# Kernel tuning notes

Measured on AMD Instinct MI355X. Metric: run time of the kernel, lower is better.

Reference implementation:

```python
import jax, jax.numpy as jnp
import numpy as np

N = 50000          # num nodes
E = 800000         # num edges (avg degree 16)
R = 8              # num relations
IN = 128
H0 = 256
H1 = 64


def _w(key, shape, fan_in):
    return jax.random.normal(key, shape, dtype=jnp.float32) * (1.0 / np.sqrt(fan_in))


def setup_inputs() -> dict:
    key = jax.random.key(0)
    ks = jax.random.split(key, 16)
    x = jax.random.normal(ks[0], (N, IN), dtype=jnp.float32)
    edge_index = jax.random.randint(ks[1], (2, E), 0, N, dtype=jnp.int64)
    edge_type = jax.random.randint(ks[2], (E,), 0, R, dtype=jnp.int64)
    return {
        "x": x,
        "edge_index": edge_index,
        "edge_type": edge_type,
        # RGCNConv params: per-relation weights [R, in, out], root weight [in, out], bias [out]
        "W1": _w(ks[3], (R, IN, H0), IN), "root1": _w(ks[4], (IN, H0), IN), "b1": jnp.zeros((H0,), jnp.float32),
        "W2": _w(ks[5], (R, H0, H0), H0), "root2": _w(ks[6], (H0, H0), H0), "b2": jnp.zeros((H0,), jnp.float32),
        "W3": _w(ks[7], (R, H0, H0), H0), "root3": _w(ks[8], (H0, H0), H0), "b3": jnp.zeros((H0,), jnp.float32),
        "W4": _w(ks[9], (R, H0, H1), H0), "root4": _w(ks[10], (H0, H1), H0), "b4": jnp.zeros((H1,), jnp.float32),
    }


def rgcn_layer(x, edge_index, edge_type, W, root, bias):
    """PyG RGCNConv: out_i = x_i @ root + sum_r (1/|N_r(i)|) sum_{j in N_r(i)} x_j @ W_r + bias.
    Aggregation is linear, so aggregate source features per (relation, dst) first,
    then apply the R small GEMMs — avoids per-edge [E, out] message materialization."""
    src, dst = edge_index[0], edge_index[1]
    seg = edge_type * N + dst                      # combined (relation, dst) segment id
    nseg = R * N
    agg = jax.ops.segment_sum(x[src], seg, num_segments=nseg)          # [R*N, in]
    cnt = jax.ops.segment_sum(jnp.ones((seg.shape[0],), x.dtype), seg, num_segments=nseg)
    agg = agg / jnp.maximum(cnt, 1.0)[:, None]                          # mean per (r, i)
    agg = agg.reshape(R, N, x.shape[1])                                 # [R, N, in]
    return jnp.einsum('rni,rio->no', agg, W) + x @ root + bias


def reference(x, edge_index, edge_type, W1, root1, b1, W2, root2, b2, W3, root3, b3, W4, root4, b4):
    h = jax.nn.relu(rgcn_layer(x, edge_index, edge_type, W1, root1, b1))
    h = jax.nn.relu(rgcn_layer(h, edge_index, edge_type, W2, root2, b2))
    h = jax.nn.relu(rgcn_layer(h, edge_index, edge_type, W3, root3, b3))
    return rgcn_layer(h, edge_index, edge_type, W4, root4, b4)
```

## Files before the change

kernel.cpp:

```cpp
#include <hip/hip_runtime.h>

#define N_NODES 50000
#define N_PAD   50048
#define N_EDGES 800000
#define N_REL   8
#define NSEG    (N_REL * N_NODES)
#define SCAN_NB 391
#define NSTRIPE 391
#define SPX     49

typedef short bf16x8 __attribute__((ext_vector_type(8)));
typedef float f32x4  __attribute__((ext_vector_type(4)));

__device__ __forceinline__ ushort f2bf(float f) {
    union { float f; unsigned u; } c; c.f = f;
    unsigned u = c.u + 0x7fffu + ((c.u >> 16) & 1u);
    return (ushort)(u >> 16);
}
__device__ __forceinline__ void add8(float* s, uint4 v) {
    unsigned u[4] = {v.x, v.y, v.z, v.w};
    #pragma unroll
    for (int k = 0; k < 4; ++k) {
        s[2 * k]     += __uint_as_float(u[k] << 16);
        s[2 * k + 1] += __uint_as_float(u[k] & 0xffff0000u);
    }
}
__device__ __forceinline__ void fma8(float* s, uint4 v, float w) {
    unsigned u[4] = {v.x, v.y, v.z, v.w};
    #pragma unroll
    for (int k = 0; k < 4; ++k) {
        s[2 * k]     = fmaf(__uint_as_float(u[k] << 16),        w, s[2 * k]);
        s[2 * k + 1] = fmaf(__uint_as_float(u[k] & 0xffff0000u), w, s[2 * k + 1]);
    }
}
__device__ __forceinline__ void async16(const ushort* g, ushort* l) {
    __builtin_amdgcn_global_load_lds((const __attribute__((address_space(1))) void*)g,
                                     (__attribute__((address_space(3))) void*)l, 16, 0, 0);
}


__global__ void count_edges(const int* __restrict__ dst, const int* __restrict__ et,
                            int* __restrict__ cnt) {
    int e = blockIdx.x * 256 + threadIdx.x;
    if (e < N_EDGES) atomicAdd(&cnt[dst[e] * N_REL + et[e]], 1);
}

__global__ __launch_bounds__(256) void scan_pass1(const int* __restrict__ cnt,
                                                  int* __restrict__ sums) {
    __shared__ int sc[256];
    int b = blockIdx.x, t = threadIdx.x;
    int base = b * 1024 + t * 4;
    int v = 0;
    #pragma unroll
    for (int i = 0; i < 4; ++i) { int idx = base + i; if (idx < NSEG) v += cnt[idx]; }
    sc[t] = v; __syncthreads();
    for (int off = 1; off < 256; off <<= 1) {
        int x = (t >= off) ? sc[t - off] : 0;
        __syncthreads(); sc[t] += x; __syncthreads();
    }
    if (t == 255) sums[b] = sc[255];
}

__global__ __launch_bounds__(512) void scan_pass2(int* __restrict__ sums, int nb) {
    __shared__ int sc[512];
    int t = threadIdx.x;
    int v = (t < nb) ? sums[t] : 0;
    sc[t] = v; __syncthreads();
    for (int off = 1; off < 512; off <<= 1) {
        int x = (t >= off) ? sc[t - off] : 0;
        __syncthreads(); sc[t] += x; __syncthreads();
    }
    if (t < nb) sums[t] = sc[t] - v;
}

__global__ __launch_bounds__(256) void scan_pass3(const int* __restrict__ cnt,
                                                  const int* __restrict__ sums,
                                                  int* __restrict__ row_ptr) {
    __shared__ int sc[256];
    int b = blockIdx.x, t = threadIdx.x;
    int base = b * 1024 + t * 4;
    int e[4]; int v = 0;
    #pragma unroll
    for (int i = 0; i < 4; ++i) { int idx = base + i; e[i] = (idx < NSEG) ? cnt[idx] : 0; v += e[i]; }
    sc[t] = v; __syncthreads();
    for (int off = 1; off < 256; off <<= 1) {
        int x = (t >= off) ? sc[t - off] : 0;
        __syncthreads(); sc[t] += x; __syncthreads();
    }
    int run = sums[b] + (sc[t] - v);
    #pragma unroll
    for (int i = 0; i < 4; ++i) {
        int idx = base + i;
        if (idx < NSEG) row_ptr[idx] = run;
        run += e[i];
    }
    if (b == 0 && t == 0) row_ptr[NSEG] = N_EDGES;
}

__global__ void place_edges(const int* __restrict__ src, const int* __restrict__ dst,
                            const int* __restrict__ et, const int* __restrict__ row_ptr,
                            int* __restrict__ cnt, int* __restrict__ sorted) {
    int e = blockIdx.x * 256 + threadIdx.x;
    if (e >= N_EDGES) return;
    int r = et[e];
    int key = dst[e] * N_REL + r;
    int old = atomicSub(&cnt[key], 1);
    int r0 = row_ptr[key];
    int c = row_ptr[key + 1] - r0;
    sorted[r0 + old - 1] = src[e] | (r << 17) | (c << 20);
}


__global__ void convert_weights(const float* __restrict__ W, const float* __restrict__ root,
                                ushort* __restrict__ BT, int K, int O, int NPAD) {
    int idx = blockIdx.x * 256 + threadIdx.x;
    if (idx >= NPAD * K) return;
    int col = idx / K, i = idx % K;
    float v = 0.0f;
    if (col < N_REL * O) {
        int r = col / O, o = col % O;
        v = W[((size_t)r * K + i) * O + o];
    } else if (col < (N_REL + 1) * O) {
        v = root[(size_t)i * O + (col - N_REL * O)];
    }
    BT[idx] = f2bf(v);
}

__global__ void f32_to_bf16(const float* __restrict__ in, ushort* __restrict__ out, int n4) {
    int i = blockIdx.x * 256 + threadIdx.x;
    if (i >= n4) return;
    float4 v = ((const float4*)in)[i];
    ushort4 s; s.x = f2bf(v.x); s.y = f2bf(v.y); s.z = f2bf(v.z); s.w = f2bf(v.w);
    ((ushort4*)out)[i] = s;
}

template<int K, int CTS, int NW>
__global__ __launch_bounds__(256)
void gemm_mfma(const ushort* __restrict__ A, const ushort* __restrict__ BT,
               ushort* __restrict__ Y) {
    const int f = blockIdx.x;
    const int g = f & 7, m = f >> 3;
    const int y = g + 8 * (m / CTS);
    const int ct = m % CTS;
    if (y >= NSTRIPE) return;
    const int row0 = y * 128;
    const int col0 = ct * 128;

    __shared__ ushort SMEM[16384];
    const int t = threadIdx.x;
    const int lane = t & 63;
    const int w = t >> 6;
    const int l16 = lane & 15, q = lane >> 4;
    const int wm = (w & 1) * 64, wn = (w >> 1) * 64;

    const int c0i = w * 64 + lane;
    const int c1i = c0i + 256;
    const int r0i = c0i >> 2, r1i = c1i >> 2;
    const int j0i = (c0i & 3) ^ ((r0i >> 1) & 3);
    const int j1i = (c1i & 3) ^ ((r1i >> 1) & 3);
    const size_t ga0 = (size_t)r0i * K + (size_t)j0i * 8;
    const size_t ga1 = (size_t)r1i * K + (size_t)j1i * 8;
    const ushort* Ab = A + (size_t)row0 * K;
    const ushort* Bb = BT + (size_t)col0 * K;

    const int qx = (q ^ ((l16 >> 1) & 3)) * 8;

    f32x4 acc[4][4] = {};

    auto STAGE = [&](int b, int k0) {
        ushort* As = SMEM + b * 8192;
        ushort* Bs = As + 4096;
        async16(Ab + k0 + ga0, &As[w * 512]);
        async16(Ab + k0 + ga1, &As[(w + 4) * 512]);
        async16(Bb + k0 + ga0, &Bs[w * 512]);
        async16(Bb + k0 + ga1, &Bs[(w + 4) * 512]);
    };
    auto COMPUTE = [&](int b) {
        ushort* As = SMEM + b * 8192;
        ushort* Bs = As + 4096;
        bf16x8 a[4], bb[4];
        #pragma unroll
        for (int i = 0; i < 4; ++i) {
            a[i]  = *(const bf16x8*)&As[(wm + i * 16 + l16) * 32 + qx];
            bb[i] = *(const bf16x8*)&Bs[(wn + i * 16 + l16) * 32 + qx];
        }
        #pragma unroll
        for (int i = 0; i < 4; ++i)
            #pragma unroll
            for (int j = 0; j < 4; ++j)
                acc[i][j] = __builtin_amdgcn_mfma_f32_16x16x32_bf16(a[i], bb[j], acc[i][j], 0, 0, 0);
    };

    constexpr int NSTEP = K / 32;
    STAGE(0, 0);
    __syncthreads();
    #pragma unroll
    for (int s = 0; s < NSTEP; ++s) {
        if (s + 1 < NSTEP) STAGE((s + 1) & 1, 32 * (s + 1));
        COMPUTE(s & 1);
        __syncthreads();
    }

    ushort* Ts = &SMEM[w * 32 * 72];
    const int rr = lane >> 3;
    const int cc = (lane & 7) * 8;
    #pragma unroll
    for (int half = 0; half < 2; ++half) {
        #pragma unroll
        for (int i = 0; i < 2; ++i)
            #pragma unroll
            for (int j = 0; j < 4; ++j)
                #pragma unroll
                for (int r = 0; r < 4; ++r)
                    Ts[(i * 16 + q * 4 + r) * 72 + j * 16 + l16] = f2bf(acc[half * 2 + i][j][r]);
        #pragma unroll
        for (int p = 0; p < 4; ++p) {
            int row = p * 8 + rr;
            uint4 v = *(const uint4*)&Ts[row * 72 + cc];
            *(uint4*)(Y + (size_t)(row0 + wm + half * 32 + row) * NW + col0 + wn + cc) = v;
        }
    }
}

template<int O>
__global__ __launch_bounds__(256)
void gather_kernel(const ushort* __restrict__ Y, int NW,
                   const int* __restrict__ row_ptr, const int* __restrict__ sorted,
                   const float* __restrict__ bias,
                   float* __restrict__ out_f32, ushort* __restrict__ out_bf16, int relu) {
    constexpr int TPN = O / 8;
    int d = blockIdx.x * (256 / TPN) + threadIdx.x / TPN;
    if (d >= N_NODES) return;
    int c0 = (threadIdx.x % TPN) * 8;
    int p0 = row_ptr[d * N_REL];
    int p1 = row_ptr[d * N_REL + N_REL];
    float sum[8] = {};
    add8(sum, *(const uint4*)(Y + (size_t)d * NW + N_REL * O + c0));
    #pragma unroll
    for (int k = 0; k < 8; ++k) sum[k] += bias[c0 + k];
    const ushort* Yc = Y + c0;
    #define EDGE_LD(sx) (*(const uint4*)(Yc + (size_t)((sx) & 0x1FFFF) * NW + ((((sx) >> 17) & 7) * O)))
    #define EDGE_W(sx)  (1.0f / (float)((unsigned)(sx) >> 20))
    int e = p0;
    for (; e + 8 <= p1; e += 8) {
        int s0 = sorted[e],     s1 = sorted[e + 1], s2 = sorted[e + 2], s3 = sorted[e + 3];
        int s4 = sorted[e + 4], s5 = sorted[e + 5], s6 = sorted[e + 6], s7 = sorted[e + 7];
        uint4 v0 = EDGE_LD(s0);
        uint4 v1 = EDGE_LD(s1);
        uint4 v2 = EDGE_LD(s2);
        uint4 v3 = EDGE_LD(s3);
        uint4 v4 = EDGE_LD(s4);
        uint4 v5 = EDGE_LD(s5);
        uint4 v6 = EDGE_LD(s6);
        uint4 v7 = EDGE_LD(s7);
        fma8(sum, v0, EDGE_W(s0));
        fma8(sum, v1, EDGE_W(s1));
        fma8(sum, v2, EDGE_W(s2));
        fma8(sum, v3, EDGE_W(s3));
        fma8(sum, v4, EDGE_W(s4));
        fma8(sum, v5, EDGE_W(s5));
        fma8(sum, v6, EDGE_W(s6));
        fma8(sum, v7, EDGE_W(s7));
    }
    if (e + 4 <= p1) {
        int s0 = sorted[e], s1 = sorted[e + 1], s2 = sorted[e + 2], s3 = sorted[e + 3];
        uint4 v0 = EDGE_LD(s0);
        uint4 v1 = EDGE_LD(s1);
        uint4 v2 = EDGE_LD(s2);
        uint4 v3 = EDGE_LD(s3);
        fma8(sum, v0, EDGE_W(s0));
        fma8(sum, v1, EDGE_W(s1));
        fma8(sum, v2, EDGE_W(s2));
        fma8(sum, v3, EDGE_W(s3));
        e += 4;
    }
    for (; e < p1; ++e) {
        int s = sorted[e];
        uint4 v = EDGE_LD(s);
        fma8(sum, v, EDGE_W(s));
    }
    #undef EDGE_LD
    #undef EDGE_W
    if (relu) {
        #pragma unroll
        for (int k = 0; k < 8; ++k) sum[k] = fmaxf(sum[k], 0.0f);
    }
    if (out_bf16) {
        ushort o[8];
        #pragma unroll
        for (int k = 0; k < 8; ++k) o[k] = f2bf(sum[k]);
        *(uint4*)(out_bf16 + (size_t)d * O + c0) = *(const uint4*)o;
    } else {
        float* p = out_f32 + (size_t)d * O + c0;
        *(float4*)p = make_float4(sum[0], sum[1], sum[2], sum[3]);
        *(float4*)(p + 4) = make_float4(sum[4], sum[5], sum[6], sum[7]);
    }
}


extern "C" void kernel_launch(void* const* d_in, const int* in_sizes, int n_in,
                              void* d_out, int out_size, void* d_ws, size_t ws_size,
                              hipStream_t stream) {
    const float* x  = (const float*)d_in[0];
    const int*   ei = (const int*)d_in[1];
    const int*   et = (const int*)d_in[2];
    const float* W[4]  = {(const float*)d_in[3], (const float*)d_in[6], (const float*)d_in[9],  (const float*)d_in[12]};
    const float* RT[4] = {(const float*)d_in[4], (const float*)d_in[7], (const float*)d_in[10], (const float*)d_in[13]};
    const float* BI[4] = {(const float*)d_in[5], (const float*)d_in[8], (const float*)d_in[11], (const float*)d_in[14]};
    const int KS[4] = {128, 256, 256, 256};
    const int NP[4] = {2304, 2304, 2304, 640};
    const int* src = ei;
    const int* dst = ei + N_EDGES;

    char* ws = (char*)d_ws;
    size_t off = 0;
    auto take = [&](size_t bytes) -> char* {
        char* p = ws + off;
        off = (off + bytes + 255) & ~(size_t)255;
        return p;
    };
    int* row_ptr    = (int*)take((size_t)(NSEG + 1) * 4);
    int* sorted     = (int*)take((size_t)N_EDGES * 4);
    ushort* BTp[4];
    for (int l = 0; l < 4; ++l) BTp[l] = (ushort*)take((size_t)NP[l] * KS[l] * 2);
    ushort* hb = (ushort*)take((size_t)N_PAD * 256 * 2);
    ushort* Yb = (ushort*)take((size_t)N_PAD * 2304 * 2);
    int* cnt  = (int*)Yb;
    int* sums = (int*)((char*)Yb + (size_t)NSEG * 4);

    hipMemsetAsync(cnt, 0, (size_t)NSEG * 4, stream);
    count_edges<<<(N_EDGES + 255) / 256, 256, 0, stream>>>(dst, et, cnt);
    scan_pass1<<<SCAN_NB, 256, 0, stream>>>(cnt, sums);
    scan_pass2<<<1, 512, 0, stream>>>(sums, SCAN_NB);
    scan_pass3<<<SCAN_NB, 256, 0, stream>>>(cnt, sums, row_ptr);
    place_edges<<<(N_EDGES + 255) / 256, 256, 0, stream>>>(src, dst, et, row_ptr, cnt, sorted);

    for (int l = 0; l < 4; ++l) {
        int n = NP[l] * KS[l];
        convert_weights<<<(n + 255) / 256, 256, 0, stream>>>(W[l], RT[l], BTp[l], KS[l],
                                                             l == 3 ? 64 : 256, NP[l]);
    }

    f32_to_bf16<<<(N_NODES * 128 / 4 + 255) / 256, 256, 0, stream>>>(x, hb, N_NODES * 128 / 4);

    const int G18 = 8 * SPX * 18;
    const int G5  = 8 * SPX * 5;
    gemm_mfma<128, 18, 2304><<<G18, 256, 0, stream>>>(hb, BTp[0], Yb);
    gather_kernel<256><<<dim3((N_NODES + 7) / 8), 256, 0, stream>>>(
        Yb, 2304, row_ptr, sorted, BI[0], nullptr, hb, 1);

    gemm_mfma<256, 18, 2304><<<G18, 256, 0, stream>>>(hb, BTp[1], Yb);
    gather_kernel<256><<<dim3((N_NODES + 7) / 8), 256, 0, stream>>>(
        Yb, 2304, row_ptr, sorted, BI[1], nullptr, hb, 1);

    gemm_mfma<256, 18, 2304><<<G18, 256, 0, stream>>>(hb, BTp[2], Yb);
    gather_kernel<256><<<dim3((N_NODES + 7) / 8), 256, 0, stream>>>(
        Yb, 2304, row_ptr, sorted, BI[2], nullptr, hb, 1);

    gemm_mfma<256, 5, 640><<<G5, 256, 0, stream>>>(hb, BTp[3], Yb);
    gather_kernel<64><<<dim3((N_NODES + 31) / 32), 256, 0, stream>>>(
        Yb, 640, row_ptr, sorted, BI[3], (float*)d_out, nullptr, 0);
}
```

Measured before the change: 666.5 us.

## Split 256-wide layers into two 128-column halves to shrink transformed intermediate

Each 256-output layer now runs as two half-width passes, each a GEMM producing a 1152-column Y (8 relations plus root for 128 outputs) followed by a gather that writes its half of the hidden state. The weights are repacked per half. Ping-pong hidden buffers replace in-place reuse. The aim is to shrink the per-pass Y buffer from 2304 to 1152 columns, so the random gather reads stay closer to cache-resident data. The cost is twice as many launches, and the GEMM rereads its A input once per half.

Result: slower. 705.7 us (+5.9%).

```diff
diff --git a/kernel.cpp b/kernel.cpp
--- a/kernel.cpp
+++ b/kernel.cpp
@@ -110,7 +110,6 @@
     sorted[r0 + old - 1] = src[e] | (r << 17) | (c << 20);
 }
 
-
 __global__ void convert_weights(const float* __restrict__ W, const float* __restrict__ root,
                                 ushort* __restrict__ BT, int K, int O, int NPAD) {
     int idx = blockIdx.x * 256 + threadIdx.x;
@@ -122,6 +121,22 @@
         v = W[((size_t)r * K + i) * O + o];
     } else if (col < (N_REL + 1) * O) {
         v = root[(size_t)i * O + (col - N_REL * O)];
+    }
+    BT[idx] = f2bf(v);
+}
+
+__global__ void convert_weights_split(const float* __restrict__ W, const float* __restrict__ root,
+                                      ushort* __restrict__ BT, int K) {
+    int idx = blockIdx.x * 256 + threadIdx.x;
+    if (idx >= 2304 * K) return;
+    int col = idx / K, i = idx % K;
+    int half = col / 1152, ch = col % 1152;
+    float v;
+    if (ch < 1024) {
+        int r = ch / 128, o = half * 128 + (ch & 127);
+        v = W[((size_t)r * K + i) * 256 + o];
+    } else {
+        v = root[(size_t)i * 256 + half * 128 + (ch - 1024)];
     }
     BT[idx] = f2bf(v);
 }
@@ -222,7 +237,7 @@
     }
 }
 
-template<int O>
+template<int O, int OSTRIDE>
 __global__ __launch_bounds__(256)
 void gather_kernel(const ushort* __restrict__ Y, int NW,
                    const int* __restrict__ row_ptr, const int* __restrict__ sorted,
@@ -289,9 +304,9 @@
         ushort o[8];
         #pragma unroll
         for (int k = 0; k < 8; ++k) o[k] = f2bf(sum[k]);
-        *(uint4*)(out_bf16 + (size_t)d * O + c0) = *(const uint4*)o;
+        *(uint4*)(out_bf16 + (size_t)d * OSTRIDE + c0) = *(const uint4*)o;
     } else {
-        float* p = out_f32 + (size_t)d * O + c0;
+        float* p = out_f32 + (size_t)d * OSTRIDE + c0;
         *(float4*)p = make_float4(sum[0], sum[1], sum[2], sum[3]);
         *(float4*)(p + 4) = make_float4(sum[4], sum[5], sum[6], sum[7]);
     }
@@ -307,8 +322,6 @@
     const float* W[4]  = {(const float*)d_in[3], (const float*)d_in[6], (const float*)d_in[9],  (const float*)d_in[12]};
     const float* RT[4] = {(const float*)d_in[4], (const float*)d_in[7], (const float*)d_in[10], (const float*)d_in[13]};
     const float* BI[4] = {(const float*)d_in[5], (const float*)d_in[8], (const float*)d_in[11], (const float*)d_in[14]};
-    const int KS[4] = {128, 256, 256, 256};
-    const int NP[4] = {2304, 2304, 2304, 640};
     const int* src = ei;
     const int* dst = ei + N_EDGES;
 
@@ -319,12 +332,16 @@
         off = (off + bytes + 255) & ~(size_t)255;
         return p;
     };
-    int* row_ptr    = (int*)take((size_t)(NSEG + 1) * 4);
-    int* sorted     = (int*)take((size_t)N_EDGES * 4);
-    ushort* BTp[4];
-    for (int l = 0; l < 4; ++l) BTp[l] = (ushort*)take((size_t)NP[l] * KS[l] * 2);
-    ushort* hb = (ushort*)take((size_t)N_PAD * 256 * 2);
-    ushort* Yb = (ushort*)take((size_t)N_PAD * 2304 * 2);
+    int* row_ptr = (int*)take((size_t)(NSEG + 1) * 4);
+    int* sorted  = (int*)take((size_t)N_EDGES * 4);
+    ushort* BT1 = (ushort*)take((size_t)2304 * 128 * 2);
+    ushort* BT2 = (ushort*)take((size_t)2304 * 256 * 2);
+    ushort* BT3 = (ushort*)take((size_t)2304 * 256 * 2);
+    ushort* BT4 = (ushort*)take((size_t)640 * 256 * 2);
+    ushort* X0  = (ushort*)take((size_t)N_PAD * 128 * 2);
+    ushort* Ha  = (ushort*)take((size_t)N_PAD * 256 * 2);
+    ushort* Hb  = (ushort*)take((size_t)N_PAD * 256 * 2);
+    ushort* Yb  = (ushort*)take((size_t)N_PAD * 1152 * 2);
     int* cnt  = (int*)Yb;
     int* sums = (int*)((char*)Yb + (size_t)NSEG * 4);
 
@@ -335,29 +352,33 @@
     scan_pass3<<<SCAN_NB, 256, 0, stream>>>(cnt, sums, row_ptr);
     place_edges<<<(N_EDGES + 255) / 256, 256, 0, stream>>>(src, dst, et, row_ptr, cnt, sorted);
 
-    for (int l = 0; l < 4; ++l) {
-        int n = NP[l] * KS[l];
-        convert_weights<<<(n + 255) / 256, 256, 0, stream>>>(W[l], RT[l], BTp[l], KS[l],
-                                                             l == 3 ? 64 : 256, NP[l]);
-    }
-
-    f32_to_bf16<<<(N_NODES * 128 / 4 + 255) / 256, 256, 0, stream>>>(x, hb, N_NODES * 128 / 4);
-
-    const int G18 = 8 * SPX * 18;
-    const int G5  = 8 * SPX * 5;
-    gemm_mfma<128, 18, 2304><<<G18, 256, 0, stream>>>(hb, BTp[0], Yb);
-    gather_kernel<256><<<dim3((N_NODES + 7) / 8), 256, 0, stream>>>(
-        Yb, 2304, row_ptr, sorted, BI[0], nullptr, hb, 1);
-
-    gemm_mfma<256, 18, 2304><<<G18, 256, 0, stream>>>(hb, BTp[1], Yb);
-    gather_kernel<256><<<dim3((N_NODES + 7) / 8), 256, 0, stream>>>(
-        Yb, 2304, row_ptr, sorted, BI[1], nullptr, hb, 1);
-
-    gemm_mfma<256, 18, 2304><<<G18, 256, 0, stream>>>(hb, BTp[2], Yb);
-    gather_kernel<256><<<dim3((N_NODES + 7) / 8), 256, 0, stream>>>(
-        Yb, 2304, row_ptr, sorted, BI[2], nullptr, hb, 1);
-
-    gemm_mfma<256, 5, 640><<<G5, 256, 0, stream>>>(hb, BTp[3], Yb);
-    gather_kernel<64><<<dim3((N_NODES + 31) / 32), 256, 0, stream>>>(
+    convert_weights_split<<<(2304 * 128 + 255) / 256, 256, 0, stream>>>(W[0], RT[0], BT1, 128);
+    convert_weights_split<<<(2304 * 256 + 255) / 256, 256, 0, stream>>>(W[1], RT[1], BT2, 256);
+    convert_weights_split<<<(2304 * 256 + 255) / 256, 256, 0, stream>>>(W[2], RT[2], BT3, 256);
+    convert_weights<<<(640 * 256 + 255) / 256, 256, 0, stream>>>(W[3], RT[3], BT4, 256, 64, 640);
+
+    f32_to_bf16<<<(N_NODES * 128 / 4 + 255) / 256, 256, 0, stream>>>(x, X0, N_NODES * 128 / 4);
+
+    const int G9 = 8 * SPX * 9;
+    const int GH = N_NODES / 16;
+
+    gemm_mfma<128, 9, 1152><<<G9, 256, 0, stream>>>(X0, BT1, Yb);
+    gather_kernel<128, 256><<<GH, 256, 0, stream>>>(Yb, 1152, row_ptr, sorted, BI[0], nullptr, Ha, 1);
+    gemm_mfma<128, 9, 1152><<<G9, 256, 0, stream>>>(X0, BT1 + (size_t)1152 * 128, Yb);
+    gather_kernel<128, 256><<<GH, 256, 0, stream>>>(Yb, 1152, row_ptr, sorted, BI[0] + 128, nullptr, Ha + 128, 1);
+
+    gemm_mfma<256, 9, 1152><<<G9, 256, 0, stream>>>(Ha, BT2, Yb);
+    gather_kernel<128, 256><<<GH, 256, 0, stream>>>(Yb, 1152, row_ptr, sorted, BI[1], nullptr, Hb, 1);
+    gemm_mfma<256, 9, 1152><<<G9, 256, 0, stream>>>(Ha, BT2 + (size_t)1152 * 256, Yb);
+    gather_kernel<128, 256><<<GH, 256, 0, stream>>>(Yb, 1152, row_ptr, sorted, BI[1] + 128, nullptr, Hb + 128, 1);
+
+    gemm_mfma<256, 9, 1152><<<G9, 256, 0, stream>>>(Hb, BT3, Yb);
+    gather_kernel<128, 256><<<GH, 256, 0, stream>>>(Yb, 1152, row_ptr, sorted, BI[2], nullptr, Ha, 1);
+    gemm_mfma<256, 9, 1152><<<G9, 256, 0, stream>>>(Hb, BT3 + (size_t)1152 * 256, Yb);
+    gather_kernel<128, 256><<<GH, 256, 0, stream>>>(Yb, 1152, row_ptr, sorted, BI[2] + 128, nullptr, Ha + 128, 1);
+
+    const int G5 = 8 * SPX * 5;
+    gemm_mfma<256, 5, 640><<<G5, 256, 0, stream>>>(Ha, BT4, Yb);
+    gather_kernel<64, 64><<<dim3((N_NODES + 31) / 32), 256, 0, stream>>>(
         Yb, 640, row_ptr, sorted, BI[3], (float*)d_out, nullptr, 0);
 }
```
